# Optimization experiments

Measured on AMD Instinct MI355X. Metric: run time of the kernel, lower is better.

The kernel has to match this reference:

```python
import jax, jax.numpy as jnp
import numpy as np

N, E = 20000, 320000
SI, VI = 128, 16          # node in dims (scalar, vector)
SE, VE = 32, 1            # edge dims
SO, VO = 64, 4            # node out dims
ANGS, RBFC = 7, 50
EPS = 1e-8
S_IN1 = 2 * SI + SE       # 288, concat [s_j, edge_s, s_i]
V_IN1 = 2 * VI + VE       # 33,  concat [v_j, edge_v, v_i]
H1 = max(V_IN1, VO)       # 33 (GVP h_dim = max(vi, vo))
H2 = max(VO, VO)          # 4


def _lin(key, din, dout):
    return jax.random.normal(key, (din, dout), jnp.float32) / np.sqrt(din)


def setup_inputs() -> dict:
    key = jax.random.key(0)
    ks = jax.random.split(key, 24)
    node_s = jax.random.normal(ks[0], (N, SI), jnp.float32)
    node_v = jax.random.normal(ks[1], (N, VI, 3), jnp.float32)
    edge_index = jax.random.randint(ks[2], (2, E), 0, N)
    edge_s = jax.random.normal(ks[3], (E, SE), jnp.float32)
    edge_v = jax.random.normal(ks[4], (E, VE, 3), jnp.float32)
    recon_mask = jax.random.bernoulli(ks[5], 0.5, (N,))
    params = dict(
        w1_wh=_lin(ks[6], V_IN1, H1),
        w1_ws=_lin(ks[7], H1 + S_IN1, SO), w1_wsb=jnp.zeros((SO,), jnp.float32),
        w1_wv=_lin(ks[8], H1, VO),
        w1_wsv=_lin(ks[9], SO, VO), w1_wsvb=jnp.zeros((VO,), jnp.float32),
        w2_wh=_lin(ks[10], VO, H2),
        w2_ws=_lin(ks[11], H2 + SO, SO), w2_wsb=jnp.zeros((SO,), jnp.float32),
        w2_wv=_lin(ks[12], H2, VO),
        w2_wsv=_lin(ks[13], SO, VO), w2_wsvb=jnp.zeros((VO,), jnp.float32),
        w3_wh=_lin(ks[14], VO, H2),
        w3_ws=_lin(ks[15], H2 + SO, SO), w3_wsb=jnp.zeros((SO,), jnp.float32),
        w3_wv=_lin(ks[16], H2, VO),
        w3_wsv=_lin(ks[17], SO, VO), w3_wsvb=jnp.zeros((VO,), jnp.float32),
    )
    return dict(node_s=node_s, node_v=node_v, edge_index=edge_index,
                edge_s=edge_s, edge_v=edge_v, recon_mask=recon_mask, **params)


def _norm_no_nan(x, axis, keepdims=False):
    return jnp.sqrt(jnp.clip(jnp.sum(x * x, axis=axis, keepdims=keepdims), 1e-8, None))


def _gvp(s, v, wh, ws, wsb, wv, wsv, wsvb, final):
    # GVP layer with vector_gate=True; activations (relu, sigmoid), or (None, None) if final.
    vt = jnp.swapaxes(v, -1, -2)            # [n, 3, vi]
    vh = vt @ wh                            # [n, 3, h]
    vn = _norm_no_nan(vh, axis=-2)          # [n, h]
    s_out = jnp.concatenate([s, vn], -1) @ ws + wsb      # [n, so]
    v_out = jnp.swapaxes(vh @ wv, -1, -2)   # [n, vo, 3]
    gate_in = s_out if final else jax.nn.sigmoid(s_out)  # vector_act(s) pre scalar_act
    gate = jax.nn.sigmoid(gate_in @ wsv + wsvb)
    v_out = v_out * gate[..., None]
    if not final:
        s_out = jax.nn.relu(s_out)
    return s_out, v_out


def reference(node_s, node_v, edge_index, edge_s, edge_v, recon_mask,
              w1_wh, w1_ws, w1_wsb, w1_wv, w1_wsv, w1_wsvb,
              w2_wh, w2_ws, w2_wsb, w2_wv, w2_wsv, w2_wsvb,
              w3_wh, w3_ws, w3_wsb, w3_wv, w3_wsv, w3_wsvb):
    src, dst = edge_index[0], edge_index[1]   # j -> i (source_to_target)
    # per-edge gather + concat: scalars [E, 2*SI+SE], vectors [E, 2*VI+VE, 3]
    s_msg = jnp.concatenate([node_s[src], edge_s, node_s[dst]], axis=-1)
    v_msg = jnp.concatenate([node_v[src], edge_v, node_v[dst]], axis=-2)
    s, v = _gvp(s_msg, v_msg, w1_wh, w1_ws, w1_wsb, w1_wv, w1_wsv, w1_wsvb, final=False)
    s, v = _gvp(s, v, w2_wh, w2_ws, w2_wsb, w2_wv, w2_wsv, w2_wsvb, final=False)
    s, v = _gvp(s, v, w3_wh, w3_ws, w3_wsb, w3_wv, w3_wsv, w3_wsvb, final=True)
    # mean aggregation at destination nodes (PyG aggr='mean'; empty nodes -> 0)
    cnt = jax.ops.segment_sum(jnp.ones((E,), s.dtype), dst, num_segments=N)
    denom = jnp.maximum(cnt, 1.0)
    s_node = jax.ops.segment_sum(s, dst, num_segments=N) / denom[:, None]
    v_node = (jax.ops.segment_sum(v.reshape(E, VO * 3), dst, num_segments=N)
              / denom[:, None]).reshape(N, VO, 3)
    # masked postprocess (original compacts via boolean indexing; we zero masked-out rows)
    m = recon_mask.astype(s_node.dtype)
    mags = jnp.linalg.norm(v_node, ord=2, axis=-1, keepdims=True)
    vectors = (v_node / (mags + EPS)) * m[:, None, None]
    scalars = jnp.concatenate([
        jnp.cos(s_node[:, :ANGS]),
        jnp.sin(s_node[:, ANGS:2 * ANGS]),
        jnp.exp(s_node[:, -RBFC:]),
    ], axis=-1) * m[:, None]
    return scalars, vectors
```

## Files before the change

kernel.cpp:

```cpp
#include <hip/hip_runtime.h>
#include <hip/hip_fp16.h>
#include <math.h>

__device__ __forceinline__ float sigm(float x) { return 1.0f / (1.0f + __expf(-x)); }

#define RANK4(XV, WPTR) do {                                                            \
    const float* w_ = (WPTR);                                                           \
    _Pragma("unroll") for (int o_ = 0; o_ < 64; ++o_) acc[o_] = fmaf((XV).x, w_[o_],       acc[o_]); \
    _Pragma("unroll") for (int o_ = 0; o_ < 64; ++o_) acc[o_] = fmaf((XV).y, w_[64 + o_],  acc[o_]); \
    _Pragma("unroll") for (int o_ = 0; o_ < 64; ++o_) acc[o_] = fmaf((XV).z, w_[128 + o_], acc[o_]); \
    _Pragma("unroll") for (int o_ = 0; o_ < 64; ++o_) acc[o_] = fmaf((XV).w, w_[192 + o_], acc[o_]); \
} while (0)

__global__ __launch_bounds__(64) void node_pre_kernel(
    const float* __restrict__ node_s, const float* __restrict__ node_v,
    const float* __restrict__ w1_wh, const float* __restrict__ w1_ws,
    float* __restrict__ ysA, float* __restrict__ ysB,
    float* __restrict__ va, float* __restrict__ vb, int N)
{
    const int oq = blockIdx.x & 3;
    const int n  = (blockIdx.x >> 2) * 64 + threadIdx.x;
    if (n >= N) return;

    float v[48];
    {
        const float4* vs = (const float4*)(node_v + (size_t)n * 48);
#pragma unroll
        for (int j = 0; j < 12; ++j) {
            float4 t = vs[j];
            v[4 * j + 0] = t.x; v[4 * j + 1] = t.y; v[4 * j + 2] = t.z; v[4 * j + 3] = t.w;
        }
    }
    const int h0 = (oq == 0) ? 0 : (1 + oq * 8);
    const int hn = (oq == 0) ? 9 : 8;
    float* vaP = va + (size_t)n * 100;
    float* vbP = vb + (size_t)n * 100;
    for (int hh = 0; hh < hn; ++hh) {
        const int h = h0 + hh;
        const float* wc = w1_wh + h;
        float a0 = 0.f, a1 = 0.f, a2 = 0.f, b0 = 0.f, b1 = 0.f, b2 = 0.f;
#pragma unroll
        for (int c = 0; c < 16; ++c) {
            const float wa = wc[c * 33];
            const float wb = wc[(17 + c) * 33];
            a0 = fmaf(v[3 * c + 0], wa, a0); a1 = fmaf(v[3 * c + 1], wa, a1); a2 = fmaf(v[3 * c + 2], wa, a2);
            b0 = fmaf(v[3 * c + 0], wb, b0); b1 = fmaf(v[3 * c + 1], wb, b1); b2 = fmaf(v[3 * c + 2], wb, b2);
        }
        vaP[3 * h + 0] = a0; vaP[3 * h + 1] = a1; vaP[3 * h + 2] = a2;
        vbP[3 * h + 0] = b0; vbP[3 * h + 1] = b1; vbP[3 * h + 2] = b2;
    }

    const float4* xs = (const float4*)(node_s + (size_t)n * 128);
    float aA[16], aB[16];
#pragma unroll
    for (int j = 0; j < 16; ++j) { aA[j] = 0.0f; aB[j] = 0.0f; }
    for (int k4 = 0; k4 < 32; ++k4) {
        float4 x = xs[k4];
        float xc[4] = {x.x, x.y, x.z, x.w};
        const float* wA = w1_ws + (size_t)(k4 * 4) * 64 + oq * 16;
        const float* wB = w1_ws + (size_t)(160 + k4 * 4) * 64 + oq * 16;
#pragma unroll
        for (int r = 0; r < 4; ++r) {
#pragma unroll
            for (int j = 0; j < 16; ++j) {
                aA[j] = fmaf(xc[r], wA[r * 64 + j], aA[j]);
                aB[j] = fmaf(xc[r], wB[r * 64 + j], aB[j]);
            }
        }
    }
    {
        float4* oa = (float4*)(ysA + (size_t)n * 64 + oq * 16);
        float4* ob = (float4*)(ysB + (size_t)n * 64 + oq * 16);
#pragma unroll
        for (int q = 0; q < 4; ++q) {
            float4 t; t.x = aA[4*q]; t.y = aA[4*q+1]; t.z = aA[4*q+2]; t.w = aA[4*q+3]; oa[q] = t;
            float4 u; u.x = aB[4*q]; u.y = aB[4*q+1]; u.z = aB[4*q+2]; u.w = aB[4*q+3]; ob[q] = u;
        }
    }
}

__global__ __launch_bounds__(64) void gvp_edge_scatter_kernel(
    const int* __restrict__ ei, const float* __restrict__ edge_s,
    const float* __restrict__ edge_v,
    const float* __restrict__ ysA, const float* __restrict__ ysB,
    const float* __restrict__ va, const float* __restrict__ vb,
    const float* __restrict__ w1_wh, const float* __restrict__ w1_ws,
    const float* __restrict__ w1_wsb, const float* __restrict__ w1_wv,
    const float* __restrict__ w1_wsv, const float* __restrict__ w1_wsvb,
    const float* __restrict__ w2_wh, const float* __restrict__ w2_ws,
    const float* __restrict__ w2_wsb, const float* __restrict__ w2_wv,
    const float* __restrict__ w2_wsv, const float* __restrict__ w2_wsvb,
    const float* __restrict__ w3_wh, const float* __restrict__ w3_ws,
    const float* __restrict__ w3_wsb, const float* __restrict__ w3_wv,
    const float* __restrict__ w3_wsv, const float* __restrict__ w3_wsvb,
    float* __restrict__ payload, int* __restrict__ slotCnt,
    int* __restrict__ slotTab, float* __restrict__ accS,
    float* __restrict__ accV, int E)
{
    __shared__ __half rows[64 * 70];
    __half* row = rows + threadIdx.x * 70;
    const int e = blockIdx.x * 64 + threadIdx.x;
    if (e >= E) return;
    const int src = ei[e];
    const int dst = ei[E + e];

    const int slot = atomicAdd(&slotCnt[dst], 1);
    if (slot < 64) slotTab[(size_t)dst * 64 + slot] = e;
    const bool ovf = (slot >= 64);

    const float ev0 = edge_v[(size_t)e * 3 + 0];
    const float ev1 = edge_v[(size_t)e * 3 + 1];
    const float ev2 = edge_v[(size_t)e * 3 + 2];

    float acc[64];
#pragma unroll
    for (int o = 0; o < 64; ++o) acc[o] = 0.0f;
    float pv[12];
#pragma unroll
    for (int i = 0; i < 12; ++i) pv[i] = 0.0f;

    const float* vaP = va + (size_t)src * 100;
    const float* vbP = vb + (size_t)dst * 100;
    for (int g = 0; g < 8; ++g) {
        float ca[12];
        {
            float4 A0 = *(const float4*)(vaP + g * 12 + 0);
            float4 A1 = *(const float4*)(vaP + g * 12 + 4);
            float4 A2 = *(const float4*)(vaP + g * 12 + 8);
            float4 B0 = *(const float4*)(vbP + g * 12 + 0);
            float4 B1 = *(const float4*)(vbP + g * 12 + 4);
            float4 B2 = *(const float4*)(vbP + g * 12 + 8);
            ca[0] = A0.x + B0.x; ca[1] = A0.y + B0.y; ca[2]  = A0.z + B0.z; ca[3]  = A0.w + B0.w;
            ca[4] = A1.x + B1.x; ca[5] = A1.y + B1.y; ca[6]  = A1.z + B1.z; ca[7]  = A1.w + B1.w;
            ca[8] = A2.x + B2.x; ca[9] = A2.y + B2.y; ca[10] = A2.z + B2.z; ca[11] = A2.w + B2.w;
        }
        const float* weP = w1_wh + 16 * 33 + 4 * g;
        const float* wvP = w1_wv + (4 * g) * 4;
        const float* wsP = w1_ws + (size_t)(288 + 4 * g) * 64;
#pragma unroll
        for (int i = 0; i < 4; ++i) {
            const float we = weP[i];
            const float d0 = ca[3 * i + 0] + ev0 * we;
            const float d1 = ca[3 * i + 1] + ev1 * we;
            const float d2 = ca[3 * i + 2] + ev2 * we;
            const float vn = sqrtf(fmaxf(d0 * d0 + d1 * d1 + d2 * d2, 1e-8f));
            const float* wr = wsP + i * 64;
#pragma unroll
            for (int o = 0; o < 64; ++o) acc[o] = fmaf(vn, wr[o], acc[o]);
#pragma unroll
            for (int vo = 0; vo < 4; ++vo) {
                const float w = wvP[i * 4 + vo];
                pv[vo * 3 + 0] = fmaf(d0, w, pv[vo * 3 + 0]);
                pv[vo * 3 + 1] = fmaf(d1, w, pv[vo * 3 + 1]);
                pv[vo * 3 + 2] = fmaf(d2, w, pv[vo * 3 + 2]);
            }
        }
    }
    {
        float4 A = *(const float4*)(vaP + 96);
        float4 B = *(const float4*)(vbP + 96);
        const float we = w1_wh[16 * 33 + 32];
        const float d0 = A.x + B.x + ev0 * we;
        const float d1 = A.y + B.y + ev1 * we;
        const float d2 = A.z + B.z + ev2 * we;
        const float vn = sqrtf(fmaxf(d0 * d0 + d1 * d1 + d2 * d2, 1e-8f));
        const float* wr = w1_ws + (size_t)320 * 64;
#pragma unroll
        for (int o = 0; o < 64; ++o) acc[o] = fmaf(vn, wr[o], acc[o]);
#pragma unroll
        for (int vo = 0; vo < 4; ++vo) {
            const float w = w1_wv[32 * 4 + vo];
            pv[vo * 3 + 0] = fmaf(d0, w, pv[vo * 3 + 0]);
            pv[vo * 3 + 1] = fmaf(d1, w, pv[vo * 3 + 1]);
            pv[vo * 3 + 2] = fmaf(d2, w, pv[vo * 3 + 2]);
        }
    }

    {
        const float4* pa = (const float4*)(ysA + (size_t)src * 64);
        const float4* pb = (const float4*)(ysB + (size_t)dst * 64);
#pragma unroll
        for (int q = 0; q < 16; ++q) {
            float4 xa = pa[q], xb = pb[q];
            acc[4 * q + 0] += xa.x + xb.x;
            acc[4 * q + 1] += xa.y + xb.y;
            acc[4 * q + 2] += xa.z + xb.z;
            acc[4 * q + 3] += xa.w + xb.w;
        }
    }
    {
        const float4* xs = (const float4*)(edge_s + (size_t)e * 32);
        for (int k4 = 0; k4 < 8; ++k4) { float4 x = xs[k4]; RANK4(x, w1_ws + (size_t)(128 + k4 * 4) * 64); }
    }

    float gp[4] = {0.f, 0.f, 0.f, 0.f};
#pragma unroll
    for (int o = 0; o < 64; ++o) {
        const float s = acc[o] + w1_wsb[o];
        const float sg = sigm(s);
#pragma unroll
        for (int vo = 0; vo < 4; ++vo) gp[vo] = fmaf(sg, w1_wsv[o * 4 + vo], gp[vo]);
        row[o] = __float2half(fmaxf(s, 0.0f));
    }
    float g1[4];
#pragma unroll
    for (int vo = 0; vo < 4; ++vo) g1[vo] = sigm(gp[vo] + w1_wsvb[vo]);
    float v1g[12];
#pragma unroll
    for (int vo = 0; vo < 4; ++vo)
#pragma unroll
        for (int d = 0; d < 3; ++d) v1g[vo * 3 + d] = pv[vo * 3 + d] * g1[vo];
    float vh2[12];
#pragma unroll
    for (int i = 0; i < 12; ++i) vh2[i] = 0.0f;
#pragma unroll
    for (int c = 0; c < 4; ++c)
#pragma unroll
        for (int h = 0; h < 4; ++h) {
            const float w = w2_wh[c * 4 + h];
#pragma unroll
            for (int d = 0; d < 3; ++d) vh2[d * 4 + h] = fmaf(v1g[c * 3 + d], w, vh2[d * 4 + h]);
        }
#pragma unroll
    for (int h = 0; h < 4; ++h) {
        const float ss = vh2[h] * vh2[h] + vh2[4 + h] * vh2[4 + h] + vh2[8 + h] * vh2[8 + h];
        row[64 + h] = __float2half(sqrtf(fmaxf(ss, 1e-8f)));
    }

    float acc2[64];
#pragma unroll
    for (int o = 0; o < 64; ++o) acc2[o] = 0.0f;
    for (int k = 0; k < 68; ++k) {
        const float xk = __half2float(row[k]);
        const float* w = w2_ws + k * 64;
#pragma unroll
        for (int o = 0; o < 64; ++o) acc2[o] = fmaf(xk, w[o], acc2[o]);
    }

    float gp2[4] = {0.f, 0.f, 0.f, 0.f};
#pragma unroll
    for (int o = 0; o < 64; ++o) {
        const float s = acc2[o] + w2_wsb[o];
        const float sg = sigm(s);
#pragma unroll
        for (int vo = 0; vo < 4; ++vo) gp2[vo] = fmaf(sg, w2_wsv[o * 4 + vo], gp2[vo]);
        row[o] = __float2half(fmaxf(s, 0.0f));
    }
    float g2[4];
#pragma unroll
    for (int vo = 0; vo < 4; ++vo) g2[vo] = sigm(gp2[vo] + w2_wsvb[vo]);
    float v2g[12];
#pragma unroll
    for (int vo = 0; vo < 4; ++vo)
#pragma unroll
        for (int d = 0; d < 3; ++d) {
            float t = 0.0f;
#pragma unroll
            for (int h = 0; h < 4; ++h) t = fmaf(vh2[d * 4 + h], w2_wv[h * 4 + vo], t);
            v2g[vo * 3 + d] = t * g2[vo];
        }
    float vh3[12];
#pragma unroll
    for (int i = 0; i < 12; ++i) vh3[i] = 0.0f;
#pragma unroll
    for (int c = 0; c < 4; ++c)
#pragma unroll
        for (int h = 0; h < 4; ++h) {
            const float w = w3_wh[c * 4 + h];
#pragma unroll
            for (int d = 0; d < 3; ++d) vh3[d * 4 + h] = fmaf(v2g[c * 3 + d], w, vh3[d * 4 + h]);
        }
#pragma unroll
    for (int h = 0; h < 4; ++h) {
        const float ss = vh3[h] * vh3[h] + vh3[4 + h] * vh3[4 + h] + vh3[8 + h] * vh3[8 + h];
        row[64 + h] = __float2half(sqrtf(fmaxf(ss, 1e-8f)));
    }

#pragma unroll
    for (int o = 0; o < 64; ++o) acc[o] = 0.0f;
    for (int k = 0; k < 68; ++k) {
        const float xk = __half2float(row[k]);
        const float* w = w3_ws + k * 64;
#pragma unroll
        for (int o = 0; o < 64; ++o) acc[o] = fmaf(xk, w[o], acc[o]);
    }

    float* P = payload + (size_t)e * 76;
    float gp3[4] = {0.f, 0.f, 0.f, 0.f};
#pragma unroll
    for (int o = 0; o < 64; ++o) {
        const float s3 = acc[o] + w3_wsb[o];
#pragma unroll
        for (int vo = 0; vo < 4; ++vo) gp3[vo] = fmaf(s3, w3_wsv[o * 4 + vo], gp3[vo]);
        P[o] = s3;
        if (ovf) atomicAdd(&accS[(size_t)dst * 64 + o], s3);
    }
    float g3[4];
#pragma unroll
    for (int vo = 0; vo < 4; ++vo) g3[vo] = sigm(gp3[vo] + w3_wsvb[vo]);
#pragma unroll
    for (int vo = 0; vo < 4; ++vo)
#pragma unroll
        for (int d = 0; d < 3; ++d) {
            float t = 0.0f;
#pragma unroll
            for (int h = 0; h < 4; ++h) t = fmaf(vh3[d * 4 + h], w3_wv[h * 4 + vo], t);
            const float val = t * g3[vo];
            P[64 + vo * 3 + d] = val;
            if (ovf) atomicAdd(&accV[(size_t)dst * 12 + vo * 3 + d], val);
        }
}

__global__ __launch_bounds__(256) void node_agg_kernel(
    const float* __restrict__ payload, const int* __restrict__ slotCnt,
    const int* __restrict__ slotTab, const float* __restrict__ accS,
    const float* __restrict__ accV, const int* __restrict__ mask,
    float* __restrict__ out, int N)
{
    const int gtid = blockIdx.x * 256 + threadIdx.x;
    const int n = gtid >> 6;
    const int lane = threadIdx.x & 63;
    if (n >= N) return;

    const int cnt = slotCnt[n];
    const int m = (cnt < 64) ? cnt : 64;

    int eid_l = (lane < m) ? slotTab[(size_t)n * 64 + lane] : 0;

    float ps[4] = {0.f, 0.f, 0.f, 0.f};
    float pvv[4] = {0.f, 0.f, 0.f, 0.f};
    for (int j = 0; j < m; j += 4) {
#pragma unroll
        for (int u = 0; u < 4; ++u) {
            const int jj = j + u;
            if (jj < m) {
                const int eid = __shfl(eid_l, jj, 64);
                const float* P = payload + (size_t)eid * 76;
                ps[u] += P[lane];
                if (lane < 12) pvv[u] += P[64 + lane];
            }
        }
    }
    float sS = (ps[0] + ps[1]) + (ps[2] + ps[3]);
    float sV = (pvv[0] + pvv[1]) + (pvv[2] + pvv[3]);
    sS += accS[(size_t)n * 64 + lane];
    if (lane < 12) sV += accV[(size_t)n * 12 + lane];

    const float denom = fmaxf((float)cnt, 1.0f);
    const float mk = (mask[n] != 0) ? 1.0f : 0.0f;

    const float s = sS / denom;
    const float r = (lane < 7) ? __cosf(s) : (lane < 14) ? __sinf(s) : __expf(s);
    out[(size_t)n * 64 + lane] = r * mk;

    const float vm = sV / denom;
    const int vo3 = (lane / 3) * 3;
    const float c0 = __shfl(vm, vo3 + 0, 64);
    const float c1 = __shfl(vm, vo3 + 1, 64);
    const float c2 = __shfl(vm, vo3 + 2, 64);
    if (lane < 12) {
        const float mag = sqrtf(c0 * c0 + c1 * c1 + c2 * c2);
        out[(size_t)N * 64 + (size_t)n * 12 + lane] = (vm / (mag + 1e-8f)) * mk;
    }
}

extern "C" void kernel_launch(void* const* d_in, const int* in_sizes, int n_in,
                              void* d_out, int out_size, void* d_ws, size_t ws_size,
                              hipStream_t stream)
{
    const float* node_s = (const float*)d_in[0];
    const float* node_v = (const float*)d_in[1];
    const int*   ei     = (const int*)d_in[2];
    const float* edge_s = (const float*)d_in[3];
    const float* edge_v = (const float*)d_in[4];
    const int*   mask   = (const int*)d_in[5];
    const float* w1_wh  = (const float*)d_in[6];
    const float* w1_ws  = (const float*)d_in[7];
    const float* w1_wsb = (const float*)d_in[8];
    const float* w1_wv  = (const float*)d_in[9];
    const float* w1_wsv = (const float*)d_in[10];
    const float* w1_wsvb= (const float*)d_in[11];
    const float* w2_wh  = (const float*)d_in[12];
    const float* w2_ws  = (const float*)d_in[13];
    const float* w2_wsb = (const float*)d_in[14];
    const float* w2_wv  = (const float*)d_in[15];
    const float* w2_wsv = (const float*)d_in[16];
    const float* w2_wsvb= (const float*)d_in[17];
    const float* w3_wh  = (const float*)d_in[18];
    const float* w3_ws  = (const float*)d_in[19];
    const float* w3_wsb = (const float*)d_in[20];
    const float* w3_wv  = (const float*)d_in[21];
    const float* w3_wsv = (const float*)d_in[22];
    const float* w3_wsvb= (const float*)d_in[23];

    const int N = in_sizes[0] / 128;
    const int E = in_sizes[3] / 32;

    float* out = (float*)d_out;
    float* ws  = (float*)d_ws;

    const size_t oYA = 0;
    const size_t oYB = (size_t)N * 64;
    const size_t oVA = oYB + (size_t)N * 64;
    const size_t oVB = oVA + (size_t)N * 100;
    const size_t oSC = oVB + (size_t)N * 100;
    const size_t oST = oSC + (size_t)N;
    const size_t oAS = oST + (size_t)N * 64;
    const size_t oAV = oAS + (size_t)N * 64;
    const size_t oPL = oAV + (size_t)N * 12;
    const size_t needF2 = oPL + (size_t)E * 76;

    if (ws_size >= needF2 * sizeof(float)) {
        int* slotCnt = (int*)(ws + oSC);
        int* slotTab = (int*)(ws + oST);
        float* accS = ws + oAS;
        float* accV = ws + oAV;
        float* payload = ws + oPL;

        hipMemsetAsync(slotCnt, 0, (size_t)N * sizeof(int), stream);
        hipMemsetAsync(accS, 0, (size_t)N * 76 * sizeof(float), stream);

        node_pre_kernel<<<((N + 63) / 64) * 4, 64, 0, stream>>>(
            node_s, node_v, w1_wh, w1_ws,
            ws + oYA, ws + oYB, ws + oVA, ws + oVB, N);
        gvp_edge_scatter_kernel<<<(E + 63) / 64, 64, 0, stream>>>(
            ei, edge_s, edge_v,
            ws + oYA, ws + oYB, ws + oVA, ws + oVB,
            w1_wh, w1_ws, w1_wsb, w1_wv, w1_wsv, w1_wsvb,
            w2_wh, w2_ws, w2_wsb, w2_wv, w2_wsv, w2_wsvb,
            w3_wh, w3_ws, w3_wsb, w3_wv, w3_wsv, w3_wsvb,
            payload, slotCnt, slotTab, accS, accV, E);
        node_agg_kernel<<<(N * 64 + 255) / 256, 256, 0, stream>>>(
            payload, slotCnt, slotTab, accS, accV, mask, out, N);
    }
}
```

Before: 521.2 us.

## Store node precomputations and edge payload in fp16 with planar vector layout

Node-side projections (ysA/ysB, va/vb) and the per-edge message payload are now stored as half precision instead of fp32, and the vector projections are laid out planar per component (stride 36) rather than interleaved. This roughly halves the bytes in the gathers of the edge kernel and the payload write and re-read in the aggregation kernel. Accumulation stays in fp32. It risks precision loss in the scalar outputs that go through exp/cos/sin, and it adds conversion instructions.

```diff
diff --git a/kernel.cpp b/kernel.cpp
--- a/kernel.cpp
+++ b/kernel.cpp
@@ -15,8 +15,8 @@
 __global__ __launch_bounds__(64) void node_pre_kernel(
     const float* __restrict__ node_s, const float* __restrict__ node_v,
     const float* __restrict__ w1_wh, const float* __restrict__ w1_ws,
-    float* __restrict__ ysA, float* __restrict__ ysB,
-    float* __restrict__ va, float* __restrict__ vb, int N)
+    __half* __restrict__ ysA, __half* __restrict__ ysB,
+    __half* __restrict__ va, __half* __restrict__ vb, int N)
 {
     const int oq = blockIdx.x & 3;
     const int n  = (blockIdx.x >> 2) * 64 + threadIdx.x;
@@ -33,8 +33,8 @@
     }
     const int h0 = (oq == 0) ? 0 : (1 + oq * 8);
     const int hn = (oq == 0) ? 9 : 8;
-    float* vaP = va + (size_t)n * 100;
-    float* vbP = vb + (size_t)n * 100;
+    __half* vaP = va + (size_t)n * 108;
+    __half* vbP = vb + (size_t)n * 108;
     for (int hh = 0; hh < hn; ++hh) {
         const int h = h0 + hh;
         const float* wc = w1_wh + h;
@@ -46,8 +46,8 @@
             a0 = fmaf(v[3 * c + 0], wa, a0); a1 = fmaf(v[3 * c + 1], wa, a1); a2 = fmaf(v[3 * c + 2], wa, a2);
             b0 = fmaf(v[3 * c + 0], wb, b0); b1 = fmaf(v[3 * c + 1], wb, b1); b2 = fmaf(v[3 * c + 2], wb, b2);
         }
-        vaP[3 * h + 0] = a0; vaP[3 * h + 1] = a1; vaP[3 * h + 2] = a2;
-        vbP[3 * h + 0] = b0; vbP[3 * h + 1] = b1; vbP[3 * h + 2] = b2;
+        vaP[0 * 36 + h] = __float2half(a0); vaP[1 * 36 + h] = __float2half(a1); vaP[2 * 36 + h] = __float2half(a2);
+        vbP[0 * 36 + h] = __float2half(b0); vbP[1 * 36 + h] = __float2half(b1); vbP[2 * 36 + h] = __float2half(b2);
     }
 
     const float4* xs = (const float4*)(node_s + (size_t)n * 128);
@@ -69,12 +69,12 @@
         }
     }
     {
-        float4* oa = (float4*)(ysA + (size_t)n * 64 + oq * 16);
-        float4* ob = (float4*)(ysB + (size_t)n * 64 + oq * 16);
-#pragma unroll
-        for (int q = 0; q < 4; ++q) {
-            float4 t; t.x = aA[4*q]; t.y = aA[4*q+1]; t.z = aA[4*q+2]; t.w = aA[4*q+3]; oa[q] = t;
-            float4 u; u.x = aB[4*q]; u.y = aB[4*q+1]; u.z = aB[4*q+2]; u.w = aB[4*q+3]; ob[q] = u;
+        __half2* oa = (__half2*)(ysA + (size_t)n * 64 + oq * 16);
+        __half2* ob = (__half2*)(ysB + (size_t)n * 64 + oq * 16);
+#pragma unroll
+        for (int q = 0; q < 8; ++q) {
+            oa[q] = __floats2half2_rn(aA[2 * q], aA[2 * q + 1]);
+            ob[q] = __floats2half2_rn(aB[2 * q], aB[2 * q + 1]);
         }
     }
 }
@@ -82,8 +82,8 @@
 __global__ __launch_bounds__(64) void gvp_edge_scatter_kernel(
     const int* __restrict__ ei, const float* __restrict__ edge_s,
     const float* __restrict__ edge_v,
-    const float* __restrict__ ysA, const float* __restrict__ ysB,
-    const float* __restrict__ va, const float* __restrict__ vb,
+    const __half* __restrict__ ysA, const __half* __restrict__ ysB,
+    const __half* __restrict__ va, const __half* __restrict__ vb,
     const float* __restrict__ w1_wh, const float* __restrict__ w1_ws,
     const float* __restrict__ w1_wsb, const float* __restrict__ w1_wv,
     const float* __restrict__ w1_wsv, const float* __restrict__ w1_wsvb,
@@ -93,7 +93,7 @@
     const float* __restrict__ w3_wh, const float* __restrict__ w3_ws,
     const float* __restrict__ w3_wsb, const float* __restrict__ w3_wv,
     const float* __restrict__ w3_wsv, const float* __restrict__ w3_wsvb,
-    float* __restrict__ payload, int* __restrict__ slotCnt,
+    __half* __restrict__ payload, int* __restrict__ slotCnt,
     int* __restrict__ slotTab, float* __restrict__ accS,
     float* __restrict__ accV, int E)
 {
@@ -119,20 +119,22 @@
 #pragma unroll
     for (int i = 0; i < 12; ++i) pv[i] = 0.0f;
 
-    const float* vaP = va + (size_t)src * 100;
-    const float* vbP = vb + (size_t)dst * 100;
+    const __half* vaP = va + (size_t)src * 108;
+    const __half* vbP = vb + (size_t)dst * 108;
     for (int g = 0; g < 8; ++g) {
         float ca[12];
-        {
-            float4 A0 = *(const float4*)(vaP + g * 12 + 0);
-            float4 A1 = *(const float4*)(vaP + g * 12 + 4);
-            float4 A2 = *(const float4*)(vaP + g * 12 + 8);
-            float4 B0 = *(const float4*)(vbP + g * 12 + 0);
-            float4 B1 = *(const float4*)(vbP + g * 12 + 4);
-            float4 B2 = *(const float4*)(vbP + g * 12 + 8);
-            ca[0] = A0.x + B0.x; ca[1] = A0.y + B0.y; ca[2]  = A0.z + B0.z; ca[3]  = A0.w + B0.w;
-            ca[4] = A1.x + B1.x; ca[5] = A1.y + B1.y; ca[6]  = A1.z + B1.z; ca[7]  = A1.w + B1.w;
-            ca[8] = A2.x + B2.x; ca[9] = A2.y + B2.y; ca[10] = A2.z + B2.z; ca[11] = A2.w + B2.w;
+#pragma unroll
+        for (int d = 0; d < 3; ++d) {
+            const __half2* pA = (const __half2*)(vaP + d * 36 + 4 * g);
+            const __half2* pB = (const __half2*)(vbP + d * 36 + 4 * g);
+            float2 a0 = __half22float2(pA[0]);
+            float2 a1 = __half22float2(pA[1]);
+            float2 b0 = __half22float2(pB[0]);
+            float2 b1 = __half22float2(pB[1]);
+            ca[0 + d] = a0.x + b0.x;
+            ca[3 + d] = a0.y + b0.y;
+            ca[6 + d] = a1.x + b1.x;
+            ca[9 + d] = a1.y + b1.y;
         }
         const float* weP = w1_wh + 16 * 33 + 4 * g;
         const float* wvP = w1_wv + (4 * g) * 4;
@@ -157,12 +159,10 @@
         }
     }
     {
-        float4 A = *(const float4*)(vaP + 96);
-        float4 B = *(const float4*)(vbP + 96);
         const float we = w1_wh[16 * 33 + 32];
-        const float d0 = A.x + B.x + ev0 * we;
-        const float d1 = A.y + B.y + ev1 * we;
-        const float d2 = A.z + B.z + ev2 * we;
+        const float d0 = __half2float(vaP[0 * 36 + 32]) + __half2float(vbP[0 * 36 + 32]) + ev0 * we;
+        const float d1 = __half2float(vaP[1 * 36 + 32]) + __half2float(vbP[1 * 36 + 32]) + ev1 * we;
+        const float d2 = __half2float(vaP[2 * 36 + 32]) + __half2float(vbP[2 * 36 + 32]) + ev2 * we;
         const float vn = sqrtf(fmaxf(d0 * d0 + d1 * d1 + d2 * d2, 1e-8f));
         const float* wr = w1_ws + (size_t)320 * 64;
 #pragma unroll
@@ -177,15 +177,14 @@
     }
 
     {
-        const float4* pa = (const float4*)(ysA + (size_t)src * 64);
-        const float4* pb = (const float4*)(ysB + (size_t)dst * 64);
-#pragma unroll
-        for (int q = 0; q < 16; ++q) {
-            float4 xa = pa[q], xb = pb[q];
-            acc[4 * q + 0] += xa.x + xb.x;
-            acc[4 * q + 1] += xa.y + xb.y;
-            acc[4 * q + 2] += xa.z + xb.z;
-            acc[4 * q + 3] += xa.w + xb.w;
+        const __half2* pa = (const __half2*)(ysA + (size_t)src * 64);
+        const __half2* pb = (const __half2*)(ysB + (size_t)dst * 64);
+#pragma unroll
+        for (int q = 0; q < 32; ++q) {
+            float2 xa = __half22float2(pa[q]);
+            float2 xb = __half22float2(pb[q]);
+            acc[2 * q + 0] += xa.x + xb.x;
+            acc[2 * q + 1] += xa.y + xb.y;
         }
     }
     {
@@ -285,19 +284,22 @@
         for (int o = 0; o < 64; ++o) acc[o] = fmaf(xk, w[o], acc[o]);
     }
 
-    float* P = payload + (size_t)e * 76;
+    __half2* P2 = (__half2*)(payload + (size_t)e * 80);
     float gp3[4] = {0.f, 0.f, 0.f, 0.f};
+    float prev = 0.0f;
 #pragma unroll
     for (int o = 0; o < 64; ++o) {
         const float s3 = acc[o] + w3_wsb[o];
 #pragma unroll
         for (int vo = 0; vo < 4; ++vo) gp3[vo] = fmaf(s3, w3_wsv[o * 4 + vo], gp3[vo]);
-        P[o] = s3;
+        if (o & 1) P2[o >> 1] = __floats2half2_rn(prev, s3);
+        else prev = s3;
         if (ovf) atomicAdd(&accS[(size_t)dst * 64 + o], s3);
     }
     float g3[4];
 #pragma unroll
     for (int vo = 0; vo < 4; ++vo) g3[vo] = sigm(gp3[vo] + w3_wsvb[vo]);
+    float v3v[12];
 #pragma unroll
     for (int vo = 0; vo < 4; ++vo)
 #pragma unroll
@@ -306,13 +308,15 @@
 #pragma unroll
             for (int h = 0; h < 4; ++h) t = fmaf(vh3[d * 4 + h], w3_wv[h * 4 + vo], t);
             const float val = t * g3[vo];
-            P[64 + vo * 3 + d] = val;
+            v3v[vo * 3 + d] = val;
             if (ovf) atomicAdd(&accV[(size_t)dst * 12 + vo * 3 + d], val);
         }
+#pragma unroll
+    for (int j = 0; j < 6; ++j) P2[32 + j] = __floats2half2_rn(v3v[2 * j], v3v[2 * j + 1]);
 }
 
 __global__ __launch_bounds__(256) void node_agg_kernel(
-    const float* __restrict__ payload, const int* __restrict__ slotCnt,
+    const __half* __restrict__ payload, const int* __restrict__ slotCnt,
     const int* __restrict__ slotTab, const float* __restrict__ accS,
     const float* __restrict__ accV, const int* __restrict__ mask,
     float* __restrict__ out, int N)
@@ -335,9 +339,9 @@
             const int jj = j + u;
             if (jj < m) {
                 const int eid = __shfl(eid_l, jj, 64);
-                const float* P = payload + (size_t)eid * 76;
-                ps[u] += P[lane];
-                if (lane < 12) pvv[u] += P[64 + lane];
+                const __half* P = payload + (size_t)eid * 80;
+                ps[u] += __half2float(P[lane]);
+                if (lane < 12) pvv[u] += __half2float(P[64 + lane]);
             }
         }
     }
@@ -400,37 +404,41 @@
     float* ws  = (float*)d_ws;
 
     const size_t oYA = 0;
-    const size_t oYB = (size_t)N * 64;
-    const size_t oVA = oYB + (size_t)N * 64;
-    const size_t oVB = oVA + (size_t)N * 100;
-    const size_t oSC = oVB + (size_t)N * 100;
-    const size_t oST = oSC + (size_t)N;
-    const size_t oAS = oST + (size_t)N * 64;
-    const size_t oAV = oAS + (size_t)N * 64;
-    const size_t oPL = oAV + (size_t)N * 12;
-    const size_t needF2 = oPL + (size_t)E * 76;
-
-    if (ws_size >= needF2 * sizeof(float)) {
+    const size_t oYB = (size_t)N * 32;
+    const size_t oVA = (size_t)N * 64;
+    const size_t oVB = (size_t)N * 118;
+    const size_t oSC = (size_t)N * 172;
+    const size_t oST = (size_t)N * 173;
+    const size_t oAS = (size_t)N * 237;
+    const size_t oAV = (size_t)N * 301;
+    const size_t oPL = (size_t)N * 313;
+    const size_t needF = oPL + (size_t)E * 40;
+
+    if (ws_size >= needF * sizeof(float)) {
+        __half* ysAH = (__half*)(ws + oYA);
+        __half* ysBH = (__half*)(ws + oYB);
+        __half* vaH  = (__half*)(ws + oVA);
+        __half* vbH  = (__half*)(ws + oVB);
         int* slotCnt = (int*)(ws + oSC);
         int* slotTab = (int*)(ws + oST);
-        float* accS = ws + oAS;
-        float* accV = ws + oAV;
-        float* payload = ws + oPL;
+        float* accS  = ws + oAS;
+        float* accV  = ws + oAV;
+        __half* payloadH = (__half*)(ws + oPL);
 
         hipMemsetAsync(slotCnt, 0, (size_t)N * sizeof(int), stream);
         hipMemsetAsync(accS, 0, (size_t)N * 76 * sizeof(float), stream);
 
         node_pre_kernel<<<((N + 63) / 64) * 4, 64, 0, stream>>>(
             node_s, node_v, w1_wh, w1_ws,
-            ws + oYA, ws + oYB, ws + oVA, ws + oVB, N);
+            ysAH, ysBH, vaH, vbH, N);
         gvp_edge_scatter_kernel<<<(E + 63) / 64, 64, 0, stream>>>(
             ei, edge_s, edge_v,
-            ws + oYA, ws + oYB, ws + oVA, ws + oVB,
+            ysAH, ysBH, vaH, vbH,
             w1_wh, w1_ws, w1_wsb, w1_wv, w1_wsv, w1_wsvb,
             w2_wh, w2_ws, w2_wsb, w2_wv, w2_wsv, w2_wsvb,
             w3_wh, w3_ws, w3_wsb, w3_wv, w3_wsv, w3_wsvb,
-            payload, slotCnt, slotTab, accS, accV, E);
+            payloadH, slotCnt, slotTab, accS, accV, E);
         node_agg_kernel<<<(N * 64 + 255) / 256, 256, 0, stream>>>(
-            payload, slotCnt, slotTab, accS, accV, mask, out, N);
+            payloadH, slotCnt, slotTab, accS, accV, mask, out, N);
     }
 }
```

Result: no change. 520.6 us (-0.1%).
